# Kernel tuning notes

Measured on AMD Instinct MI355X. Metric: run time of the kernel, lower is better.

The kernel has to match this reference:

```python
import jax, jax.numpy as jnp
import numpy as np

N_NODES = 50000
N_EDGES = 800000
D_NODE = 64
D_EDGE_IN = 64
D_EDGE_OUT = 64
D_NODE_OUT = 64
HIDDEN = [128, 128, 128]


def _mlp_params(key, in_c, out_c, hidden):
    dims = [in_c] + hidden + [out_c]
    ws, bs = [], []
    for i in range(len(dims) - 1):
        key, k1 = jax.random.split(key)
        ws.append(jax.random.normal(k1, (dims[i], dims[i + 1]), dtype=jnp.float32) * 0.05)
        bs.append(jnp.zeros((dims[i + 1],), dtype=jnp.float32))
    return ws, bs, key


def _mlp(x, ws, bs):
    # Linear -> ReLU for all but last layer, final Linear has no activation
    for w, b in zip(ws[:-1], bs[:-1]):
        x = jax.nn.relu(x @ w + b)
    return x @ ws[-1] + bs[-1]


def setup_inputs() -> dict:
    key = jax.random.key(0)
    k1, k2, k3, key = jax.random.split(key, 4)
    h = jax.random.normal(k1, (N_NODES, D_NODE), dtype=jnp.float32)
    edge_index = jax.random.randint(k2, (2, N_EDGES), 0, N_NODES, dtype=jnp.int64)
    edge_attr = jax.random.normal(k3, (N_EDGES, D_EDGE_IN), dtype=jnp.float32)
    ews, ebs, key = _mlp_params(key, 2 * D_NODE + D_EDGE_IN, D_EDGE_OUT, HIDDEN)
    nws, nbs, key = _mlp_params(key, D_NODE + D_EDGE_OUT, D_NODE_OUT, HIDDEN)
    inp = {"h": h, "edge_index": edge_index, "edge_attr": edge_attr}
    for i in range(4):
        inp[f"ew{i}"] = ews[i]
        inp[f"eb{i}"] = ebs[i]
        inp[f"nw{i}"] = nws[i]
        inp[f"nb{i}"] = nbs[i]
    return inp


def reference(h, edge_index, edge_attr,
              ew0, eb0, ew1, eb1, ew2, eb2, ew3, eb3,
              nw0, nb0, nw1, nb1, nw2, nb2, nw3, nb3):
    row, col = edge_index[0], edge_index[1]
    # EdgeUpdate: gather endpoints, concat with edge_attr, MLP
    edge_in = jnp.concatenate([h[row], h[col], edge_attr], axis=-1)  # [E, 192]
    edge_out = _mlp(edge_in, [ew0, ew1, ew2, ew3], [eb0, eb1, eb2, eb3])  # [E, 64]
    # NodeUpdate: scatter-add messages (message = edge_attr) to target nodes (col)
    msg = jax.ops.segment_sum(edge_out, col, num_segments=h.shape[0])  # [N, 64]
    node_in = jnp.concatenate([h, msg], axis=-1)  # [N, 128]
    h_out = _mlp(node_in, [nw0, nw1, nw2, nw3], [nb0, nb1, nb2, nb3])  # [N, 64]
    return (h_out, edge_out)
```

## Files before the change

### kernel.cpp

```cpp
#include <hip/hip_runtime.h>

#define E_TOTAL 800000
#define NN 50000
#define MSG_BYTES (NN * 64 * 4)

typedef unsigned short u16;
typedef short short8 __attribute__((ext_vector_type(8)));
typedef float floatx4 __attribute__((ext_vector_type(4)));

__device__ __forceinline__ u16 f2bf(float f) {
    union { float f; unsigned int i; } x; x.f = f;
    unsigned int i = x.i;
    return (u16)((i + 0x7FFFu + ((i >> 16) & 1u)) >> 16);
}
__device__ __forceinline__ unsigned int pack2(float a, float b) {
    return (unsigned int)f2bf(a) | ((unsigned int)f2bf(b) << 16);
}
__device__ __forceinline__ uint2 cvt4(const float* p) {
    float4 v = *(const float4*)p;
    uint2 r; r.x = pack2(v.x, v.y); r.y = pack2(v.z, v.w);
    return r;
}

template<int K, int N, bool RELU>
__device__ __forceinline__ void layer_slab(const u16* lds_in, int in_stride,
                                           u16* lds_out, int out_stride,
                                           const u16* __restrict__ wt,
                                           const float* __restrict__ bias,
                                           int lane)
{
    const int m = lane & 15, quad = lane >> 4;
    short8 a[K / 32];
#pragma unroll
    for (int kb = 0; kb < K / 32; ++kb)
        a[kb] = *(const short8*)(lds_in + m * in_stride + kb * 32 + quad * 8);
#pragma unroll
    for (int nt = 0; nt < N / 16; nt += 2) {
        floatx4 acc0 = {0.f, 0.f, 0.f, 0.f}, acc1 = {0.f, 0.f, 0.f, 0.f};
        const int n0 = nt * 16 + m, n1 = n0 + 16;
        const u16* w0 = wt + n0 * K + quad * 8;
        const u16* w1 = wt + n1 * K + quad * 8;
#pragma unroll
        for (int kb = 0; kb < K / 32; ++kb) {
            short8 b0 = *(const short8*)(w0 + kb * 32);
            short8 b1 = *(const short8*)(w1 + kb * 32);
            acc0 = __builtin_amdgcn_mfma_f32_16x16x32_bf16(a[kb], b0, acc0, 0, 0, 0);
            acc1 = __builtin_amdgcn_mfma_f32_16x16x32_bf16(a[kb], b1, acc1, 0, 0, 0);
        }
        float bb0 = bias[n0], bb1 = bias[n1];
#pragma unroll
        for (int r = 0; r < 4; ++r) {
            int row = quad * 4 + r;
            float v0 = acc0[r] + bb0, v1 = acc1[r] + bb1;
            if (RELU) { v0 = fmaxf(v0, 0.f); v1 = fmaxf(v1, 0.f); }
            lds_out[row * out_stride + n0] = f2bf(v0);
            lds_out[row * out_stride + n1] = f2bf(v1);
        }
    }
}

__global__ __launch_bounds__(256) void prep_wt(
    const float* __restrict__ e0, const float* __restrict__ e1,
    const float* __restrict__ e2, const float* __restrict__ e3,
    const float* __restrict__ m0, const float* __restrict__ m1,
    const float* __restrict__ m2, const float* __restrict__ m3,
    u16* __restrict__ dst)
{
    int t = blockIdx.x * 256 + threadIdx.x;
    if (t >= 122880) return;
    const int offs[9] = {0, 24576, 40960, 57344, 65536, 81920, 98304, 114688, 122880};
    const int Ks[8]   = {192, 128, 128, 128, 128, 128, 128, 128};
    const int Ns[8]   = {128, 128, 128,  64, 128, 128, 128,  64};
    const float* srcs[8] = {e0, e1, e2, e3, m0, m1, m2, m3};
    int s = 0;
    while (t >= offs[s + 1]) ++s;
    int e = t - offs[s];
    int K = Ks[s], N = Ns[s];
    int n = e / K, k = e - n * K;
    dst[t] = f2bf(srcs[s][k * N + n]);
}

__global__ __launch_bounds__(256) void edge_kernel(
    const float* __restrict__ h, const int* __restrict__ eidx,
    const float* __restrict__ ea, const u16* __restrict__ wt,
    const float* __restrict__ eb0, const float* __restrict__ eb1,
    const float* __restrict__ eb2, const float* __restrict__ eb3,
    float* __restrict__ msg, float* __restrict__ out_edge)
{
    __shared__ u16 Xs[64 * 200];
    __shared__ u16 Ha[64 * 136];
    __shared__ u16 Hb[64 * 136];
    __shared__ int row_s[64], col_s[64];

    const int tid = threadIdx.x;
    const int ebase = blockIdx.x * 64;

    if (tid < 64)       row_s[tid] = eidx[ebase + tid];
    else if (tid < 128) col_s[tid - 64] = eidx[E_TOTAL + ebase + (tid - 64)];
    __syncthreads();

#pragma unroll
    for (int g = tid; g < 1024; g += 256) {
        int e = g >> 4, c = g & 15;
        *(uint2*)&Xs[e * 200 + c * 4] = cvt4(h + (size_t)row_s[e] * 64 + c * 4);
    }
#pragma unroll
    for (int g = tid; g < 1024; g += 256) {
        int e = g >> 4, c = g & 15;
        *(uint2*)&Xs[e * 200 + 64 + c * 4] = cvt4(h + (size_t)col_s[e] * 64 + c * 4);
    }
#pragma unroll
    for (int g = tid; g < 1024; g += 256) {
        int e = g >> 4, c = g & 15;
        *(uint2*)&Xs[e * 200 + 128 + c * 4] = cvt4(ea + (size_t)(ebase + e) * 64 + c * 4);
    }
    __syncthreads();

    const int wave = tid >> 6, lane = tid & 63;
    const int w16 = wave * 16;
    const u16* wtE0 = wt;
    const u16* wtE1 = wt + 24576;
    const u16* wtE2 = wt + 40960;
    const u16* wtE3 = wt + 57344;

    layer_slab<192, 128, true>(Xs + w16 * 200, 200, Ha + w16 * 136, 136, wtE0, eb0, lane);
    layer_slab<128, 128, true>(Ha + w16 * 136, 136, Hb + w16 * 136, 136, wtE1, eb1, lane);
    layer_slab<128, 128, true>(Hb + w16 * 136, 136, Ha + w16 * 136, 136, wtE2, eb2, lane);

    {
        const u16* in = Ha + w16 * 136;
        const int m = lane & 15, quad = lane >> 4;
        short8 a[4];
#pragma unroll
        for (int kb = 0; kb < 4; ++kb)
            a[kb] = *(const short8*)(in + m * 136 + kb * 32 + quad * 8);
#pragma unroll
        for (int np = 0; np < 2; ++np) {
            floatx4 acc0 = {0, 0, 0, 0}, acc1 = {0, 0, 0, 0};
            const int n0 = np * 32 + m, n1 = n0 + 16;
#pragma unroll
            for (int kb = 0; kb < 4; ++kb) {
                short8 b0 = *(const short8*)(wtE3 + n0 * 128 + kb * 32 + quad * 8);
                short8 b1 = *(const short8*)(wtE3 + n1 * 128 + kb * 32 + quad * 8);
                acc0 = __builtin_amdgcn_mfma_f32_16x16x32_bf16(a[kb], b0, acc0, 0, 0, 0);
                acc1 = __builtin_amdgcn_mfma_f32_16x16x32_bf16(a[kb], b1, acc1, 0, 0, 0);
            }
            float bb0 = eb3[n0], bb1 = eb3[n1];
#pragma unroll
            for (int r = 0; r < 4; ++r) {
                int rl = w16 + quad * 4 + r;
                size_t e = (size_t)(ebase + rl);
                float v0 = acc0[r] + bb0, v1 = acc1[r] + bb1;
                out_edge[e * 64 + n0] = v0;
                out_edge[e * 64 + n1] = v1;
                float* mrow = msg + (size_t)col_s[rl] * 64;
                atomicAdd(mrow + n0, v0);
                atomicAdd(mrow + n1, v1);
            }
        }
    }
}

__global__ __launch_bounds__(256) void node_kernel(
    const float* __restrict__ h, const float* __restrict__ msg,
    const u16* __restrict__ wt,
    const float* __restrict__ nb0, const float* __restrict__ nb1,
    const float* __restrict__ nb2, const float* __restrict__ nb3,
    float* __restrict__ out_node)
{
    __shared__ u16 Xs[64 * 136];
    __shared__ u16 Ha[64 * 136];
    __shared__ u16 Hb[64 * 136];

    const int tid = threadIdx.x;
    const int nbase = blockIdx.x * 64;

#pragma unroll
    for (int g = tid; g < 1024; g += 256) {
        int e = g >> 4, c = g & 15;
        int node = nbase + e;
        uint2 v = {0u, 0u};
        if (node < NN) v = cvt4(h + (size_t)node * 64 + c * 4);
        *(uint2*)&Xs[e * 136 + c * 4] = v;
    }
#pragma unroll
    for (int g = tid; g < 1024; g += 256) {
        int e = g >> 4, c = g & 15;
        int node = nbase + e;
        uint2 v = {0u, 0u};
        if (node < NN) v = cvt4(msg + (size_t)node * 64 + c * 4);
        *(uint2*)&Xs[e * 136 + 64 + c * 4] = v;
    }
    __syncthreads();

    const int wave = tid >> 6, lane = tid & 63;
    const int w16 = wave * 16;
    const u16* wtN0 = wt + 65536;
    const u16* wtN1 = wt + 81920;
    const u16* wtN2 = wt + 98304;
    const u16* wtN3 = wt + 114688;

    layer_slab<128, 128, true>(Xs + w16 * 136, 136, Ha + w16 * 136, 136, wtN0, nb0, lane);
    layer_slab<128, 128, true>(Ha + w16 * 136, 136, Hb + w16 * 136, 136, wtN1, nb1, lane);
    layer_slab<128, 128, true>(Hb + w16 * 136, 136, Ha + w16 * 136, 136, wtN2, nb2, lane);

    {
        const u16* in = Ha + w16 * 136;
        const int m = lane & 15, quad = lane >> 4;
        short8 a[4];
#pragma unroll
        for (int kb = 0; kb < 4; ++kb)
            a[kb] = *(const short8*)(in + m * 136 + kb * 32 + quad * 8);
#pragma unroll
        for (int np = 0; np < 2; ++np) {
            floatx4 acc0 = {0, 0, 0, 0}, acc1 = {0, 0, 0, 0};
            const int n0 = np * 32 + m, n1 = n0 + 16;
#pragma unroll
            for (int kb = 0; kb < 4; ++kb) {
                short8 b0 = *(const short8*)(wtN3 + n0 * 128 + kb * 32 + quad * 8);
                short8 b1 = *(const short8*)(wtN3 + n1 * 128 + kb * 32 + quad * 8);
                acc0 = __builtin_amdgcn_mfma_f32_16x16x32_bf16(a[kb], b0, acc0, 0, 0, 0);
                acc1 = __builtin_amdgcn_mfma_f32_16x16x32_bf16(a[kb], b1, acc1, 0, 0, 0);
            }
            float bb0 = nb3[n0], bb1 = nb3[n1];
#pragma unroll
            for (int r = 0; r < 4; ++r) {
                int rl = w16 + quad * 4 + r;
                int node = nbase + rl;
                if (node < NN) {
                    out_node[(size_t)node * 64 + n0] = acc0[r] + bb0;
                    out_node[(size_t)node * 64 + n1] = acc1[r] + bb1;
                }
            }
        }
    }
}

extern "C" void kernel_launch(void* const* d_in, const int* in_sizes, int n_in,
                              void* d_out, int out_size, void* d_ws, size_t ws_size,
                              hipStream_t stream)
{
    const float* h   = (const float*)d_in[0];
    const int* eidx  = (const int*)d_in[1];
    const float* ea  = (const float*)d_in[2];
    const float* ew0 = (const float*)d_in[3];
    const float* eb0 = (const float*)d_in[4];
    const float* nw0 = (const float*)d_in[5];
    const float* nb0 = (const float*)d_in[6];
    const float* ew1 = (const float*)d_in[7];
    const float* eb1 = (const float*)d_in[8];
    const float* nw1 = (const float*)d_in[9];
    const float* nb1 = (const float*)d_in[10];
    const float* ew2 = (const float*)d_in[11];
    const float* eb2 = (const float*)d_in[12];
    const float* nw2 = (const float*)d_in[13];
    const float* nb2 = (const float*)d_in[14];
    const float* ew3 = (const float*)d_in[15];
    const float* eb3 = (const float*)d_in[16];
    const float* nw3 = (const float*)d_in[17];
    const float* nb3 = (const float*)d_in[18];

    float* msg = (float*)d_ws;
    u16* wt    = (u16*)((char*)d_ws + MSG_BYTES);
    float* out_node = (float*)d_out;
    float* out_edge = out_node + (size_t)NN * 64;

    hipMemsetAsync(d_ws, 0, MSG_BYTES, stream);
    prep_wt<<<480, 256, 0, stream>>>(ew0, ew1, ew2, ew3, nw0, nw1, nw2, nw3, wt);
    edge_kernel<<<E_TOTAL / 64, 256, 0, stream>>>(h, eidx, ea, wt,
                                                  eb0, eb1, eb2, eb3, msg, out_edge);
    node_kernel<<<(NN + 63) / 64, 256, 0, stream>>>(h, msg, wt,
                                                    nb0, nb1, nb2, nb3, out_node);
}
```

Baseline: 1.164 ms.

## Replace atomic scatter-add with CSR gather of edge outputs in node kernel

Removes the per-element float atomicAdds into the message buffer from the edge kernel. In their place, a histogram, a single-block scan and a fill kernel build a CSR list of incoming edges per target node, and the node kernel gathers and sums edge_out rows directly. It also reuses the input LDS buffer as a ping-pong buffer to cut shared memory per block, which may raise occupancy. The cost is three extra launches, a serial single-block scan, a re-read of edge_out, and fill atomics that make the summation order nondeterministic.

New measurement: 1.334 ms. 1.15x slower.

```diff
diff --git a/kernel.cpp b/kernel.cpp
--- a/kernel.cpp
+++ b/kernel.cpp
@@ -2,7 +2,8 @@
 
 #define E_TOTAL 800000
 #define NN 50000
-#define MSG_BYTES (NN * 64 * 4)
+#define WT_U16 122880
+#define WT_BYTES (WT_U16 * 2)
 
 typedef unsigned short u16;
 typedef short short8 __attribute__((ext_vector_type(8)));
@@ -19,6 +20,10 @@
 __device__ __forceinline__ uint2 cvt4(const float* p) {
     float4 v = *(const float4*)p;
     uint2 r; r.x = pack2(v.x, v.y); r.y = pack2(v.z, v.w);
+    return r;
+}
+__device__ __forceinline__ uint2 packf4(floatx4 v) {
+    uint2 r; r.x = pack2(v[0], v[1]); r.y = pack2(v[2], v[3]);
     return r;
 }
 
@@ -67,7 +72,7 @@
     u16* __restrict__ dst)
 {
     int t = blockIdx.x * 256 + threadIdx.x;
-    if (t >= 122880) return;
+    if (t >= WT_U16) return;
     const int offs[9] = {0, 24576, 40960, 57344, 65536, 81920, 98304, 114688, 122880};
     const int Ks[8]   = {192, 128, 128, 128, 128, 128, 128, 128};
     const int Ns[8]   = {128, 128, 128,  64, 128, 128, 128,  64};
@@ -80,16 +85,62 @@
     dst[t] = f2bf(srcs[s][k * N + n]);
 }
 
+__global__ __launch_bounds__(256) void hist_kernel(const int* __restrict__ eidx,
+                                                   int* __restrict__ deg)
+{
+    int e = blockIdx.x * 256 + threadIdx.x;
+    if (e < E_TOTAL) atomicAdd(&deg[eidx[E_TOTAL + e]], 1);
+}
+
+__global__ __launch_bounds__(256) void scan_kernel(const int* __restrict__ deg,
+                                                   int* __restrict__ off,
+                                                   int* __restrict__ cur)
+{
+    __shared__ int sums[256];
+    const int t = threadIdx.x;
+    const int CH = (NN + 255) / 256;
+    int s0 = t * CH, s1 = s0 + CH;
+    if (s0 > NN) s0 = NN;
+    if (s1 > NN) s1 = NN;
+    int sum = 0;
+    for (int i = s0; i < s1; ++i) sum += deg[i];
+    sums[t] = sum;
+    __syncthreads();
+    for (int d = 1; d < 256; d <<= 1) {
+        int v = (t >= d) ? sums[t - d] : 0;
+        __syncthreads();
+        sums[t] += v;
+        __syncthreads();
+    }
+    int base = (t == 0) ? 0 : sums[t - 1];
+    for (int i = s0; i < s1; ++i) {
+        off[i] = base; cur[i] = base;
+        base += deg[i];
+    }
+    if (t == 255) off[NN] = sums[255];
+}
+
+__global__ __launch_bounds__(256) void fill_kernel(const int* __restrict__ eidx,
+                                                   int* __restrict__ cur,
+                                                   int* __restrict__ eid)
+{
+    int e = blockIdx.x * 256 + threadIdx.x;
+    if (e < E_TOTAL) {
+        int c = eidx[E_TOTAL + e];
+        int p = atomicAdd(&cur[c], 1);
+        eid[p] = e;
+    }
+}
+
 __global__ __launch_bounds__(256) void edge_kernel(
     const float* __restrict__ h, const int* __restrict__ eidx,
     const float* __restrict__ ea, const u16* __restrict__ wt,
     const float* __restrict__ eb0, const float* __restrict__ eb1,
     const float* __restrict__ eb2, const float* __restrict__ eb3,
-    float* __restrict__ msg, float* __restrict__ out_edge)
+    float* __restrict__ out_edge)
 {
     __shared__ u16 Xs[64 * 200];
     __shared__ u16 Ha[64 * 136];
-    __shared__ u16 Hb[64 * 136];
     __shared__ int row_s[64], col_s[64];
 
     const int tid = threadIdx.x;
@@ -124,8 +175,8 @@
     const u16* wtE3 = wt + 57344;
 
     layer_slab<192, 128, true>(Xs + w16 * 200, 200, Ha + w16 * 136, 136, wtE0, eb0, lane);
-    layer_slab<128, 128, true>(Ha + w16 * 136, 136, Hb + w16 * 136, 136, wtE1, eb1, lane);
-    layer_slab<128, 128, true>(Hb + w16 * 136, 136, Ha + w16 * 136, 136, wtE2, eb2, lane);
+    layer_slab<128, 128, true>(Ha + w16 * 136, 136, Xs + w16 * 200, 200, wtE1, eb1, lane);
+    layer_slab<128, 128, true>(Xs + w16 * 200, 200, Ha + w16 * 136, 136, wtE2, eb2, lane);
 
     {
         const u16* in = Ha + w16 * 136;
@@ -150,19 +201,16 @@
             for (int r = 0; r < 4; ++r) {
                 int rl = w16 + quad * 4 + r;
                 size_t e = (size_t)(ebase + rl);
-                float v0 = acc0[r] + bb0, v1 = acc1[r] + bb1;
-                out_edge[e * 64 + n0] = v0;
-                out_edge[e * 64 + n1] = v1;
-                float* mrow = msg + (size_t)col_s[rl] * 64;
-                atomicAdd(mrow + n0, v0);
-                atomicAdd(mrow + n1, v1);
+                out_edge[e * 64 + n0] = acc0[r] + bb0;
+                out_edge[e * 64 + n1] = acc1[r] + bb1;
             }
         }
     }
 }
 
 __global__ __launch_bounds__(256) void node_kernel(
-    const float* __restrict__ h, const float* __restrict__ msg,
+    const float* __restrict__ h, const float* __restrict__ edge_out,
+    const int* __restrict__ off, const int* __restrict__ eid,
     const u16* __restrict__ wt,
     const float* __restrict__ nb0, const float* __restrict__ nb1,
     const float* __restrict__ nb2, const float* __restrict__ nb3,
@@ -170,7 +218,6 @@
 {
     __shared__ u16 Xs[64 * 136];
     __shared__ u16 Ha[64 * 136];
-    __shared__ u16 Hb[64 * 136];
 
     const int tid = threadIdx.x;
     const int nbase = blockIdx.x * 64;
@@ -183,13 +230,24 @@
         if (node < NN) v = cvt4(h + (size_t)node * 64 + c * 4);
         *(uint2*)&Xs[e * 136 + c * 4] = v;
     }
-#pragma unroll
-    for (int g = tid; g < 1024; g += 256) {
-        int e = g >> 4, c = g & 15;
-        int node = nbase + e;
-        uint2 v = {0u, 0u};
-        if (node < NN) v = cvt4(msg + (size_t)node * 64 + c * 4);
-        *(uint2*)&Xs[e * 136 + 64 + c * 4] = v;
+    {
+        const int row = tid >> 2, p = tid & 3;
+        const int node = nbase + row;
+        floatx4 a0 = {0, 0, 0, 0}, a1 = {0, 0, 0, 0};
+        floatx4 a2 = {0, 0, 0, 0}, a3 = {0, 0, 0, 0};
+        if (node < NN) {
+            int s = off[node], e1 = off[node + 1];
+            for (int j = s; j < e1; ++j) {
+                const floatx4* src =
+                    (const floatx4*)(edge_out + (size_t)eid[j] * 64 + p * 16);
+                a0 += src[0]; a1 += src[1]; a2 += src[2]; a3 += src[3];
+            }
+        }
+        u16* dst = Xs + row * 136 + 64 + p * 16;
+        ((uint2*)dst)[0] = packf4(a0);
+        ((uint2*)dst)[1] = packf4(a1);
+        ((uint2*)dst)[2] = packf4(a2);
+        ((uint2*)dst)[3] = packf4(a3);
     }
     __syncthreads();
 
@@ -201,8 +259,8 @@
     const u16* wtN3 = wt + 114688;
 
     layer_slab<128, 128, true>(Xs + w16 * 136, 136, Ha + w16 * 136, 136, wtN0, nb0, lane);
-    layer_slab<128, 128, true>(Ha + w16 * 136, 136, Hb + w16 * 136, 136, wtN1, nb1, lane);
-    layer_slab<128, 128, true>(Hb + w16 * 136, 136, Ha + w16 * 136, 136, wtN2, nb2, lane);
+    layer_slab<128, 128, true>(Ha + w16 * 136, 136, Xs + w16 * 136, 136, wtN1, nb1, lane);
+    layer_slab<128, 128, true>(Xs + w16 * 136, 136, Ha + w16 * 136, 136, wtN2, nb2, lane);
 
     {
         const u16* in = Ha + w16 * 136;
@@ -260,15 +318,22 @@
     const float* nw3 = (const float*)d_in[17];
     const float* nb3 = (const float*)d_in[18];
 
-    float* msg = (float*)d_ws;
-    u16* wt    = (u16*)((char*)d_ws + MSG_BYTES);
+    u16* wt  = (u16*)d_ws;
+    int* deg = (int*)((char*)d_ws + WT_BYTES);
+    int* off = deg + NN;
+    int* cur = off + NN + 1;
+    int* eid = cur + NN + 1;
+
     float* out_node = (float*)d_out;
     float* out_edge = out_node + (size_t)NN * 64;
 
-    hipMemsetAsync(d_ws, 0, MSG_BYTES, stream);
+    hipMemsetAsync(deg, 0, NN * sizeof(int), stream);
     prep_wt<<<480, 256, 0, stream>>>(ew0, ew1, ew2, ew3, nw0, nw1, nw2, nw3, wt);
+    hist_kernel<<<(E_TOTAL + 255) / 256, 256, 0, stream>>>(eidx, deg);
+    scan_kernel<<<1, 256, 0, stream>>>(deg, off, cur);
+    fill_kernel<<<(E_TOTAL + 255) / 256, 256, 0, stream>>>(eidx, cur, eid);
     edge_kernel<<<E_TOTAL / 64, 256, 0, stream>>>(h, eidx, ea, wt,
-                                                  eb0, eb1, eb2, eb3, msg, out_edge);
-    node_kernel<<<(NN + 63) / 64, 256, 0, stream>>>(h, msg, wt,
+                                                  eb0, eb1, eb2, eb3, out_edge);
+    node_kernel<<<(NN + 63) / 64, 256, 0, stream>>>(h, out_edge, off, eid, wt,
                                                     nb0, nb1, nb2, nb3, out_node);
 }
```
